# Optimization experiments

Measured on AMD Instinct MI355X. Metric: run time of the kernel, lower is better.

Reference implementation:

```python
import jax, jax.numpy as jnp
import numpy as np

N, C, H, W = 4, 128, 128, 128
G, K, PAD, DIL = 4, 3, 1, 1
P = K * K
HID = 4 * C
EPS = 1e-6


def ln(x, w, b):
    m = jnp.mean(x, -1, keepdims=True)
    v = jnp.mean((x - m) ** 2, -1, keepdims=True)
    return (x - m) * jax.lax.rsqrt(v + EPS) * w + b


def linear(x, w, b):
    return x @ w.T + b


def grid_sample_zeros(img, grid):
    # img: (B,Hi,Wi,Cc); grid: (B,L,P,2) xy in [-1,1]; bilinear, zeros padding, align_corners=False
    B, Hi, Wi, Cc = img.shape
    gx = (grid[..., 0] + 1.0) * (Wi * 0.5) - 0.5
    gy = (grid[..., 1] + 1.0) * (Hi * 0.5) - 0.5
    x0 = jnp.floor(gx)
    y0 = jnp.floor(gy)
    wx1 = gx - x0
    wy1 = gy - y0
    flat = img.reshape(B, Hi * Wi, Cc)
    Bq, L, Pq = gx.shape

    def tap(yy, xx, wgt):
        valid = (xx >= 0) & (xx <= Wi - 1) & (yy >= 0) & (yy <= Hi - 1)
        idx = (jnp.clip(yy, 0, Hi - 1) * Wi + jnp.clip(xx, 0, Wi - 1)).astype(jnp.int32)
        v = jnp.take_along_axis(flat, idx.reshape(B, L * Pq)[..., None], axis=1)
        return v.reshape(B, L, Pq, Cc) * (wgt * valid)[..., None]

    return (tap(y0, x0, (1 - wx1) * (1 - wy1))
            + tap(y0, x0 + 1, wx1 * (1 - wy1))
            + tap(y0 + 1, x0, (1 - wx1) * wy1)
            + tap(y0 + 1, x0 + 1, wx1 * wy1))


def dcn_core(x, offset, mask):
    # faithful port of dcnv3_core_pytorch (stride=1, offset_scale=1.0)
    n, h, w, c = x.shape
    gc = c // G
    xp = jnp.pad(x, ((0, 0), (PAD, PAD), (PAD, PAD), (0, 0)))
    hi, wi = h + 2 * PAD, w + 2 * PAD
    base = (DIL * (K - 1)) // 2 + 0.5
    ref_y = (base + jnp.arange(h, dtype=jnp.float32)) / hi
    ref_x = (base + jnp.arange(w, dtype=jnp.float32)) / wi
    ref = jnp.stack([jnp.broadcast_to(ref_x[None, :], (h, w)),
                     jnp.broadcast_to(ref_y[:, None], (h, w))], -1)  # (h,w,2) xy
    ks = jnp.arange(K, dtype=jnp.float32) * DIL - (DIL * (K - 1)) // 2
    gxk, gyk = jnp.meshgrid(ks, ks, indexing='ij')  # x slow, y fast (torch meshgrid order)
    grid = jnp.tile(jnp.stack([gxk / wi, gyk / hi], -1).reshape(P, 2), (G, 1))  # (G*P,2)
    sn = jnp.array([wi, hi], jnp.float32)
    loc = ref[None, :, :, None, :] + grid[None, None, None] + offset.reshape(n, h, w, G * P, 2) / sn
    sg = (2.0 * loc - 1.0).reshape(n, h * w, G, P, 2).transpose(0, 2, 1, 3, 4).reshape(n * G, h * w, P, 2)
    img = xp.reshape(n, hi, wi, G, gc).transpose(0, 3, 1, 2, 4).reshape(n * G, hi, wi, gc)
    samp = grid_sample_zeros(img, sg)  # (n*G, h*w, P, gc)
    m = mask.reshape(n, h * w, G, P).transpose(0, 2, 1, 3).reshape(n * G, h * w, P)
    out = jnp.einsum('blpc,blp->blc', samp, m)
    return out.reshape(n, G, h * w, gc).transpose(0, 2, 1, 3).reshape(n, h, w, c)


def dcn_forward(xcl, dw_w, dw_b, dwln_w, dwln_b, off_w, off_b, mask_w, mask_b, outproj_w, outproj_b):
    n, h, w, c = xcl.shape
    y = jax.lax.conv_general_dilated(xcl.transpose(0, 3, 1, 2), dw_w, (1, 1),
                                     ((PAD, PAD), (PAD, PAD)),
                                     dimension_numbers=('NCHW', 'OIHW', 'NCHW'),
                                     feature_group_count=C)
    y = y + dw_b[None, :, None, None]
    x1 = jax.nn.gelu(ln(y.transpose(0, 2, 3, 1), dwln_w, dwln_b), approximate=False)
    offset = linear(x1, off_w, off_b)
    m = jax.nn.softmax(linear(x1, mask_w, mask_b).reshape(n, h, w, G, P), -1).reshape(n, h, w, G * P)
    out = dcn_core(x1, offset, m)
    return linear(out, outproj_w, outproj_b)


def setup_inputs():
    key = jax.random.key(0)
    ks = jax.random.split(key, 8)
    s = 0.02
    return {
        "x": jax.random.normal(ks[0], (N, C, H, W), jnp.float32),
        "norm1_w": jnp.ones((C,), jnp.float32), "norm1_b": jnp.zeros((C,), jnp.float32),
        "dw_w": jax.random.normal(ks[1], (C, 1, K, K), jnp.float32) * 0.1,
        "dw_b": jnp.zeros((C,), jnp.float32),
        "dwln_w": jnp.ones((C,), jnp.float32), "dwln_b": jnp.zeros((C,), jnp.float32),
        "off_w": jax.random.normal(ks[2], (G * P * 2, C), jnp.float32) * 0.05,
        "off_b": jax.random.normal(ks[3], (G * P * 2,), jnp.float32) * 0.5,
        "mask_w": jax.random.normal(ks[4], (G * P, C), jnp.float32) * 0.05,
        "mask_b": jnp.zeros((G * P,), jnp.float32),
        "outproj_w": jax.random.normal(ks[5], (C, C), jnp.float32) * s,
        "outproj_b": jnp.zeros((C,), jnp.float32),
        "norm2_w": jnp.ones((C,), jnp.float32), "norm2_b": jnp.zeros((C,), jnp.float32),
        "fc1_w": jax.random.normal(ks[6], (HID, C), jnp.float32) * s,
        "fc1_b": jnp.zeros((HID,), jnp.float32),
        "fc2_w": jax.random.normal(ks[7], (C, HID), jnp.float32) * s,
        "fc2_b": jnp.zeros((C,), jnp.float32),
    }


def reference(x, norm1_w, norm1_b, dw_w, dw_b, dwln_w, dwln_b, off_w, off_b,
              mask_w, mask_b, outproj_w, outproj_b, norm2_w, norm2_b,
              fc1_w, fc1_b, fc2_w, fc2_b):
    # pre-norm branch (layer_scale=None, post_norm=False, res_post_norm=False, drop_path=Identity)
    xcl = ln(x.transpose(0, 2, 3, 1), norm1_w, norm1_b)  # channels_first -> channels_last LN
    d = dcn_forward(xcl, dw_w, dw_b, dwln_w, dwln_b, off_w, off_b, mask_w, mask_b, outproj_w, outproj_b)
    x = x + d.transpose(0, 3, 1, 2)
    y = ln(x.transpose(0, 2, 3, 1), norm2_w, norm2_b)
    y = linear(jax.nn.gelu(linear(y, fc1_w, fc1_b), approximate=False), fc2_w, fc2_b)
    return x + y.transpose(0, 3, 1, 2)
```

## Files before the change

kernel.cpp:

```cpp
#include <hip/hip_runtime.h>

typedef unsigned short ushort_t;
typedef short short8 __attribute__((ext_vector_type(8)));
typedef float f32x4 __attribute__((ext_vector_type(4)));
typedef ushort_t ushort8v __attribute__((ext_vector_type(8)));
typedef ushort_t ushort4v __attribute__((ext_vector_type(4)));

#define HWsz 16384
#define NHWsz 65536
#define YS 136

__device__ __forceinline__ float b2f(ushort_t u){ return __uint_as_float(((unsigned)u)<<16); }
__device__ __forceinline__ ushort_t f2b(float f){
  unsigned x = __float_as_uint(f);
  x += 0x7fffu + ((x>>16)&1u);
  return (ushort_t)(x>>16);
}
__device__ __forceinline__ float gelu_fast(float x){
  float t = x*x;
  float e = __expf(x*(1.5957691216f + 0.0713548163f*t));
  return x - x*__builtin_amdgcn_rcpf(1.0f + e);
}

#define HSW(p, b) ((p)*1024 + ((b) ^ (((p)&7)<<4)))
#define XSW(p, b) ((p)*256  + ((b) ^ (((p)&7)<<4)))

__global__ __launch_bounds__(256) void kW_cvt(const float* __restrict__ w1, const float* __restrict__ w2,
    const float* __restrict__ offw, const float* __restrict__ maskw, const float* __restrict__ dww,
    const float* __restrict__ pw, const float* __restrict__ offb, const float* __restrict__ mb,
    ushort_t* __restrict__ w1b, ushort_t* __restrict__ w2b, ushort_t* __restrict__ owmb,
    float* __restrict__ dwwT, ushort_t* __restrict__ pwh, ushort_t* __restrict__ pwl,
    float* __restrict__ obm){
  int i = blockIdx.x*256 + threadIdx.x;
  w1b[i] = f2b(w1[i]);
  w2b[i] = f2b(w2[i]);
  if (i < 16384){
    int row = i >> 7, k = i & 127;
    float v = 0.f;
    if (row < 72) v = offw[row*128 + k];
    else if (row < 108) v = maskw[(row-72)*128 + k];
    owmb[i] = f2b(v);
    float pv = pw[i];
    ushort_t hi = f2b(pv);
    pwh[i] = hi;
    pwl[i] = f2b(pv - b2f(hi));
  }
  if (i < 1152){
    int k = i >> 7, c = i & 127;
    dwwT[i] = dww[c*9 + k];
  }
  if (i < 128){
    obm[i] = (i < 72) ? offb[i] : ((i < 108) ? mb[i-72] : 0.f);
  }
}

__global__ __launch_bounds__(256) void kA_ln1(const float* __restrict__ x,
    const float* __restrict__ w, const float* __restrict__ b,
    ushort_t* __restrict__ xcl){
  __shared__ float tile[128*66];
  __shared__ float psum[256], psq[256];
  __shared__ float ms[64], rs[64];
  int t = threadIdx.x;
  int pos0 = blockIdx.x * 64;
  int n = pos0 >> 14, hw0 = pos0 & 16383;
  const float* xb = x + (size_t)n*128*HWsz + hw0;
  for (int i=0;i<32;i++){
    int e = i*256+t;
    int c = e>>6, p = e&63;
    tile[c*66+p] = xb[(size_t)c*HWsz + p];
  }
  __syncthreads();
  {
    int part = t>>6, p = t&63;
    float s=0.f, q=0.f;
    for (int c=part*32; c<part*32+32; c++){ float v = tile[c*66+p]; s+=v; q+=v*v; }
    psum[part*64+p]=s; psq[part*64+p]=q;
  }
  __syncthreads();
  if (t<64){
    float s=psum[t]+psum[64+t]+psum[128+t]+psum[192+t];
    float q=psq[t]+psq[64+t]+psq[128+t]+psq[192+t];
    float m = s*(1.0f/128.0f);
    float v = q*(1.0f/128.0f)-m*m;
    ms[t]=m; rs[t]=rsqrtf(v+1e-6f);
  }
  __syncthreads();
  for (int i=0;i<32;i++){
    int e = i*256+t;
    int p = e>>7, c = e&127;
    float v = (tile[c*66+p]-ms[p])*rs[p]*w[c]+b[c];
    xcl[(size_t)(pos0+p)*128 + c] = f2b(v);
  }
}

__global__ __launch_bounds__(256) void kB_dw(const ushort_t* __restrict__ xcl,
    const float* __restrict__ dwwT, const float* __restrict__ dwb,
    const float* __restrict__ lnw, const float* __restrict__ lnb,
    ushort_t* __restrict__ x1){
  __shared__ float partS[16*17], partQ[16*17];
  __shared__ float ms[16], rs[16];
  int t = threadIdx.x;
  int pos0 = blockIdx.x*16;
  int n = pos0>>14, hw0 = pos0&16383, h = hw0>>7, w0 = hw0&127;
  int pp = t>>4, l = t&15, ch0 = l*8;
  int w = w0 + pp;
  float acc[8];
  {
    float4 b0 = *(const float4*)(dwb + ch0);
    float4 b1 = *(const float4*)(dwb + ch0 + 4);
    acc[0]=b0.x; acc[1]=b0.y; acc[2]=b0.z; acc[3]=b0.w;
    acc[4]=b1.x; acc[5]=b1.y; acc[6]=b1.z; acc[7]=b1.w;
  }
  #pragma unroll
  for (int kh=0; kh<3; kh++){
    int hy = h + kh - 1;
    if ((unsigned)hy < 128u){
      #pragma unroll
      for (int kw=0; kw<3; kw++){
        int wx = w + kw - 1;
        if ((unsigned)wx < 128u){
          ushort8v xv = *(const ushort8v*)(xcl + ((size_t)(n*16384 + hy*128 + wx))*128 + ch0);
          const float* wr = dwwT + (kh*3+kw)*128 + ch0;
          float4 w0v = *(const float4*)(wr);
          float4 w1v = *(const float4*)(wr+4);
          acc[0] += b2f(xv[0])*w0v.x; acc[1] += b2f(xv[1])*w0v.y;
          acc[2] += b2f(xv[2])*w0v.z; acc[3] += b2f(xv[3])*w0v.w;
          acc[4] += b2f(xv[4])*w1v.x; acc[5] += b2f(xv[5])*w1v.y;
          acc[6] += b2f(xv[6])*w1v.z; acc[7] += b2f(xv[7])*w1v.w;
        }
      }
    }
  }
  {
    float s=0.f, q=0.f;
    #pragma unroll
    for (int j=0;j<8;j++){ s+=acc[j]; q+=acc[j]*acc[j]; }
    partS[pp*17+l]=s; partQ[pp*17+l]=q;
  }
  __syncthreads();
  if (t<16){
    float s=0.f, q=0.f;
    for (int i=0;i<16;i++){ s += partS[t*17+i]; q += partQ[t*17+i]; }
    float m = s*(1.0f/128.0f);
    float var = q*(1.0f/128.0f) - m*m;
    ms[t]=m; rs[t]=rsqrtf(var+1e-6f);
  }
  __syncthreads();
  {
    float m = ms[pp], r = rs[pp];
    float4 lw0 = *(const float4*)(lnw + ch0);
    float4 lw1 = *(const float4*)(lnw + ch0 + 4);
    float4 lb0 = *(const float4*)(lnb + ch0);
    float4 lb1 = *(const float4*)(lnb + ch0 + 4);
    float lw[8] = {lw0.x,lw0.y,lw0.z,lw0.w,lw1.x,lw1.y,lw1.z,lw1.w};
    float lb[8] = {lb0.x,lb0.y,lb0.z,lb0.w,lb1.x,lb1.y,lb1.z,lb1.w};
    ushort8v o;
    #pragma unroll
    for (int j=0;j<8;j++){
      float v = (acc[j]-m)*r*lw[j]+lb[j];
      o[j] = f2b(gelu_fast(v));
    }
    *(ushort8v*)(x1 + (size_t)(pos0+pp)*128 + ch0) = o;
  }
}

#define RS 120
__global__ __launch_bounds__(256) void kCD_dcn(const ushort_t* __restrict__ x1,
    const ushort_t* __restrict__ owmb, const float* __restrict__ obm,
    ushort_t* __restrict__ dcnout){
  __shared__ __align__(16) ushort_t xLb[16*YS];
  __shared__ float raw[16*RS];
  __shared__ __align__(16) float descW[576*4];
  __shared__ __align__(16) int   descO[576*4];
  int t = threadIdx.x;
  int pos0 = blockIdx.x*16;
  int n = pos0>>14, hw0 = pos0&16383, h = hw0>>7, w0 = hw0&127;
  const size_t imgbase = (size_t)n*16384*128;

  *(ushort8v*)(xLb + (t>>4)*YS + (t&15)*8) = *(const ushort8v*)(x1 + (size_t)pos0*128 + t*8);
  __syncthreads();

  {
    int wave = t>>6, lane = t&63;
    int ma = lane&15, quad = lane>>4;
    short8 afrag[4];
    #pragma unroll
    for (int ks=0; ks<4; ks++)
      afrag[ks] = *(const short8*)(xLb + ma*YS + ks*32 + quad*8);
    f32x4 acc[2];
    acc[0] = (f32x4){0.f,0.f,0.f,0.f};
    acc[1] = (f32x4){0.f,0.f,0.f,0.f};
    #pragma unroll
    for (int tile=0; tile<2; tile++){
      const ushort_t* brow = owmb + (size_t)(wave*32 + tile*16 + ma)*128 + quad*8;
      #pragma unroll
      for (int ks=0; ks<4; ks++){
        short8 bfrag = *(const short8*)(brow + ks*32);
        acc[tile] = __builtin_amdgcn_mfma_f32_16x16x32_bf16(bfrag, afrag[ks], acc[tile], 0,0,0);
      }
    }
    #pragma unroll
    for (int tile=0; tile<2; tile++){
      int row0 = wave*32 + tile*16 + quad*4;
      if (row0 < 112){
        f32x4 bias4 = *(const f32x4*)(obm + row0);
        f32x4 o;
        #pragma unroll
        for (int r=0;r<4;r++) o[r] = acc[tile][r] + bias4[r];
        *(f32x4*)(raw + ma*RS + row0) = o;
      }
    }
  }
  __syncthreads();

  if (t < 64){
    int p = t>>2, g = t&3;
    float* mr = raw + p*RS + 72 + g*9;
    float mx = -1e30f;
    for (int q=0;q<9;q++) mx = fmaxf(mx, mr[q]);
    float e[9]; float ssum=0.f;
    for (int q=0;q<9;q++){ e[q]=expf(mr[q]-mx); ssum+=e[q]; }
    float inv = 1.0f/ssum;
    for (int q=0;q<9;q++) mr[q] = e[q]*inv;
  }
  __syncthreads();

  for (int it=0; it<3; it++){
    int tid = t + 256*it;
    if (tid < 576){
      int pp = tid/36, rem = tid - pp*36;
      int g = rem/9, p = rem - g*9;
      int i = p/3, j = p - i*3;
      float ox = raw[pp*RS + 2*(g*9+p)];
      float oy = raw[pp*RS + 2*(g*9+p)+1];
      float mval = raw[pp*RS + 72 + g*9 + p];
      float px = (float)(w0 + pp + i - 1) + ox;
      float py = (float)(h + j - 1) + oy;
      float fx0 = floorf(px), fy0 = floorf(py);
      int ix0 = (int)fx0, iy0 = (int)fy0;
      float fx = px - fx0, fy = py - fy0;
      float vx0 = ((unsigned)ix0     < 128u) ? 1.f : 0.f;
      float vx1 = ((unsigned)(ix0+1) < 128u) ? 1.f : 0.f;
      float vy0 = ((unsigned)iy0     < 128u) ? 1.f : 0.f;
      float vy1 = ((unsigned)(iy0+1) < 128u) ? 1.f : 0.f;
      int cx0 = min(max(ix0,0),127), cx1 = min(max(ix0+1,0),127);
      int cy0 = min(max(iy0,0),127), cy1 = min(max(iy0+1,0),127);
      float4 wv;
      wv.x = (1.f-fx)*(1.f-fy)*mval*vx0*vy0;
      wv.y = fx*(1.f-fy)*mval*vx1*vy0;
      wv.z = (1.f-fx)*fy*mval*vx0*vy1;
      wv.w = fx*fy*mval*vx1*vy1;
      int4 ov;
      ov.x = (cy0*128+cx0)*128;
      ov.y = (cy0*128+cx1)*128;
      ov.z = (cy1*128+cx0)*128;
      ov.w = (cy1*128+cx1)*128;
      *(float4*)(descW + tid*4) = wv;
      *(int4*)(descO + tid*4) = ov;
    }
  }
  __syncthreads();

  {
    int pp = t>>4, l = t&15;
    int ch0 = l*8, g = l>>2;
    const ushort_t* ib = x1 + imgbase + ch0;
    float acc[8];
    #pragma unroll
    for (int j=0;j<8;j++) acc[j]=0.f;
    int dbase = pp*36 + g*9;
    #pragma unroll
    for (int p=0;p<9;p++){
      float4 wv = *(const float4*)(descW + (dbase+p)*4);
      int4  ov = *(const int4*)(descO + (dbase+p)*4);
      ushort8v v00 = *(const ushort8v*)(ib + ov.x);
      ushort8v v10 = *(const ushort8v*)(ib + ov.y);
      ushort8v v01 = *(const ushort8v*)(ib + ov.z);
      ushort8v v11 = *(const ushort8v*)(ib + ov.w);
      #pragma unroll
      for (int j=0;j<8;j++){
        float s = wv.x*b2f(v00[j]) + wv.y*b2f(v10[j]) + wv.z*b2f(v01[j]) + wv.w*b2f(v11[j]);
        acc[j] += s;
      }
    }
    ushort8v outv;
    #pragma unroll
    for (int j=0;j<8;j++) outv[j] = f2b(acc[j]);
    *(ushort8v*)(dcnout + (size_t)(pos0+pp)*128 + ch0) = outv;
  }
}

__global__ __launch_bounds__(256, 4) void kEFG(const ushort_t* __restrict__ dcnout,
    const ushort_t* __restrict__ pwh, const ushort_t* __restrict__ pwl,
    const float* __restrict__ pb, const float* __restrict__ x,
    const float* __restrict__ n2w, const float* __restrict__ n2b,
    const ushort_t* __restrict__ w1b, const float* __restrict__ b1,
    const ushort_t* __restrict__ w2b, const float* __restrict__ b2,
    float* __restrict__ out){
  __shared__ __align__(16) char hidb[32*1024];
  __shared__ __align__(16) char xnb[32*256];
  float* partS = (float*)hidb;
  float* partQ = partS + 32*17;
  float* msh   = partQ + 32*17;
  float* rsh   = msh + 32;

  int t = threadIdx.x;
  int pos0 = blockIdx.x*32;
  int n = pos0>>14, hw0 = pos0&16383;
  int wave = t>>6, lane = t&63;
  int ma = lane&15, quad = lane>>4;

  short8 af[2][4];
  #pragma unroll
  for (int mt=0; mt<2; mt++)
    #pragma unroll
    for (int ks=0; ks<4; ks++)
      af[mt][ks] = *(const short8*)(dcnout + (size_t)(pos0+mt*16+ma)*128 + ks*32 + quad*8);

  f32x4 acc[2][2];
  #pragma unroll
  for (int i=0;i<2;i++){ acc[i][0]=(f32x4){0.f,0.f,0.f,0.f}; acc[i][1]=(f32x4){0.f,0.f,0.f,0.f}; }
  #pragma unroll
  for (int tile=0; tile<2; tile++){
    int c0 = wave*32 + tile*16;
    const ushort_t* bh = pwh + (size_t)(c0 + ma)*128 + quad*8;
    const ushort_t* bl = pwl + (size_t)(c0 + ma)*128 + quad*8;
    #pragma unroll
    for (int ks=0; ks<4; ks++){
      short8 bfh = *(const short8*)(bh + ks*32);
      short8 bfl = *(const short8*)(bl + ks*32);
      #pragma unroll
      for (int mt=0; mt<2; mt++){
        acc[tile][mt] = __builtin_amdgcn_mfma_f32_16x16x32_bf16(bfh, af[mt][ks], acc[tile][mt], 0,0,0);
        acc[tile][mt] = __builtin_amdgcn_mfma_f32_16x16x32_bf16(bfl, af[mt][ks], acc[tile][mt], 0,0,0);
      }
    }
  }

  float vb[2][2][4];
  float sAcc[2], qAcc[2];
  sAcc[0]=0.f; sAcc[1]=0.f; qAcc[0]=0.f; qAcc[1]=0.f;
  #pragma unroll
  for (int tile=0; tile<2; tile++){
    int c0 = wave*32 + tile*16 + quad*4;
    f32x4 bias4 = *(const f32x4*)(pb + c0);
    #pragma unroll
    for (int mt=0; mt<2; mt++){
      int p = mt*16 + ma;
      #pragma unroll
      for (int r=0;r<4;r++){
        float res = x[((size_t)(n*128) + c0 + r)*HWsz + hw0 + p];
        float v = acc[tile][mt][r] + bias4[r] + res;
        float vv = b2f(f2b(v));
        vb[tile][mt][r] = vv;
        sAcc[mt] += vv; qAcc[mt] += vv*vv;
      }
    }
  }
  #pragma unroll
  for (int mt=0; mt<2; mt++){
    int p = mt*16 + ma;
    partS[p*17 + wave*4 + quad] = sAcc[mt];
    partQ[p*17 + wave*4 + quad] = qAcc[mt];
  }
  __syncthreads();
  if (t < 32){
    float s=0.f, q=0.f;
    for (int i=0;i<16;i++){ s += partS[t*17+i]; q += partQ[t*17+i]; }
    float m = s*(1.0f/128.0f);
    float var = q*(1.0f/128.0f) - m*m;
    msh[t] = m; rsh[t] = rsqrtf(var+1e-6f);
  }
  __syncthreads();

  #pragma unroll
  for (int tile=0; tile<2; tile++){
    int c0 = wave*32 + tile*16 + quad*4;
    f32x4 w4 = *(const f32x4*)(n2w + c0);
    f32x4 b4 = *(const f32x4*)(n2b + c0);
    #pragma unroll
    for (int mt=0; mt<2; mt++){
      int p = mt*16 + ma;
      float m = msh[p], r = rsh[p];
      ushort4v nv;
      #pragma unroll
      for (int rr=0;rr<4;rr++) nv[rr] = f2b((vb[tile][mt][rr]-m)*r*w4[rr] + b4[rr]);
      *(ushort4v*)(xnb + XSW(p, c0*2)) = nv;
    }
  }
  __syncthreads();

  short8 axf[2][4];
  #pragma unroll
  for (int ks=0; ks<4; ks++)
    #pragma unroll
    for (int mt=0; mt<2; mt++)
      axf[mt][ks] = *(const short8*)(xnb + XSW(mt*16+ma, ks*64 + quad*16));

  int nbase = wave*128;
  short8 wcur[4], wnxt[4];
  {
    const ushort_t* brow = w1b + (size_t)(nbase + ma)*128 + quad*8;
    #pragma unroll
    for (int ks=0; ks<4; ks++) wcur[ks] = *(const short8*)(brow + ks*32);
  }
  #pragma unroll
  for (int tile=0; tile<8; tile++){
    if (tile < 7){
      const ushort_t* brow = w1b + (size_t)(nbase + (tile+1)*16 + ma)*128 + quad*8;
      #pragma unroll
      for (int ks=0; ks<4; ks++) wnxt[ks] = *(const short8*)(brow + ks*32);
    }
    f32x4 a0 = (f32x4){0.f,0.f,0.f,0.f};
    f32x4 a1 = (f32x4){0.f,0.f,0.f,0.f};
    #pragma unroll
    for (int ks=0; ks<4; ks++){
      a0 = __builtin_amdgcn_mfma_f32_16x16x32_bf16(wcur[ks], axf[0][ks], a0, 0,0,0);
      a1 = __builtin_amdgcn_mfma_f32_16x16x32_bf16(wcur[ks], axf[1][ks], a1, 0,0,0);
    }
    int n0 = nbase + tile*16 + quad*4;
    f32x4 bias4 = *(const f32x4*)(b1 + n0);
    ushort4v hv0, hv1;
    #pragma unroll
    for (int r=0;r<4;r++){
      hv0[r] = f2b(gelu_fast(a0[r] + bias4[r]));
      hv1[r] = f2b(gelu_fast(a1[r] + bias4[r]));
    }
    *(ushort4v*)(hidb + HSW(ma,    n0*2)) = hv0;
    *(ushort4v*)(hidb + HSW(16+ma, n0*2)) = hv1;
    #pragma unroll
    for (int ks=0; ks<4; ks++) wcur[ks] = wnxt[ks];
  }
  __syncthreads();

  f32x4 acc2[2][2];
  acc2[0][0]=(f32x4){0.f,0.f,0.f,0.f}; acc2[0][1]=(f32x4){0.f,0.f,0.f,0.f};
  acc2[1][0]=(f32x4){0.f,0.f,0.f,0.f}; acc2[1][1]=(f32x4){0.f,0.f,0.f,0.f};
  const ushort_t* wb0 = w2b + (size_t)(wave*32 + ma)*512 + quad*8;
  const ushort_t* wb1 = w2b + (size_t)(wave*32 + 16 + ma)*512 + quad*8;
  short8 hc0 = *(const short8*)(hidb + HSW(ma,    quad*16));
  short8 hc1 = *(const short8*)(hidb + HSW(16+ma, quad*16));
  short8 wc0 = *(const short8*)(wb0);
  short8 wc1 = *(const short8*)(wb1);
  #pragma unroll
  for (int ks=0; ks<16; ks++){
    short8 hn0, hn1, wn0, wn1;
    if (ks < 15){
      hn0 = *(const short8*)(hidb + HSW(ma,    (ks+1)*64 + quad*16));
      hn1 = *(const short8*)(hidb + HSW(16+ma, (ks+1)*64 + quad*16));
      wn0 = *(const short8*)(wb0 + (ks+1)*32);
      wn1 = *(const short8*)(wb1 + (ks+1)*32);
    }
    acc2[0][0] = __builtin_amdgcn_mfma_f32_16x16x32_bf16(wc0, hc0, acc2[0][0], 0,0,0);
    acc2[0][1] = __builtin_amdgcn_mfma_f32_16x16x32_bf16(wc0, hc1, acc2[0][1], 0,0,0);
    acc2[1][0] = __builtin_amdgcn_mfma_f32_16x16x32_bf16(wc1, hc0, acc2[1][0], 0,0,0);
    acc2[1][1] = __builtin_amdgcn_mfma_f32_16x16x32_bf16(wc1, hc1, acc2[1][1], 0,0,0);
    if (ks < 15){ hc0=hn0; hc1=hn1; wc0=wn0; wc1=wn1; }
  }

  #pragma unroll
  for (int tile=0; tile<2; tile++){
    int c0 = wave*32 + tile*16 + quad*4;
    f32x4 bias4 = *(const f32x4*)(b2 + c0);
    #pragma unroll
    for (int mt=0; mt<2; mt++){
      int p = mt*16 + ma;
      #pragma unroll
      for (int r=0;r<4;r++){
        float v = acc2[tile][mt][r] + bias4[r] + vb[tile][mt][r];
        out[((size_t)(n*128) + c0 + r)*HWsz + hw0 + p] = v;
      }
    }
  }
}

extern "C" void kernel_launch(void* const* d_in, const int* in_sizes, int n_in,
                              void* d_out, int out_size, void* d_ws, size_t ws_size,
                              hipStream_t stream){
  const float* x     = (const float*)d_in[0];
  const float* n1w   = (const float*)d_in[1];
  const float* n1b   = (const float*)d_in[2];
  const float* dww   = (const float*)d_in[3];
  const float* dwb   = (const float*)d_in[4];
  const float* dwlnw = (const float*)d_in[5];
  const float* dwlnb = (const float*)d_in[6];
  const float* offw  = (const float*)d_in[7];
  const float* offb  = (const float*)d_in[8];
  const float* maskw = (const float*)d_in[9];
  const float* maskb = (const float*)d_in[10];
  const float* pw    = (const float*)d_in[11];
  const float* pb    = (const float*)d_in[12];
  const float* n2w   = (const float*)d_in[13];
  const float* n2b   = (const float*)d_in[14];
  const float* w1    = (const float*)d_in[15];
  const float* b1    = (const float*)d_in[16];
  const float* w2    = (const float*)d_in[17];
  const float* b2    = (const float*)d_in[18];

  char* wsb = (char*)d_ws;
  ushort_t* R0   = (ushort_t*)(wsb);
  ushort_t* R1   = (ushort_t*)(wsb + (16u<<20));
  ushort_t* w1b  = (ushort_t*)(wsb + (32u<<20));
  ushort_t* w2b  = (ushort_t*)(wsb + (32u<<20) + (128u<<10));
  ushort_t* owmb = (ushort_t*)(wsb + (32u<<20) + (256u<<10));
  ushort_t* pwh  = (ushort_t*)(wsb + (32u<<20) + (288u<<10));
  ushort_t* pwl  = (ushort_t*)(wsb + (32u<<20) + (320u<<10));
  float*    dwwT = (float*)(wsb + (32u<<20) + (352u<<10));
  float*    obm  = (float*)(wsb + (32u<<20) + (358u<<10));
  float* out = (float*)d_out;

  hipLaunchKernelGGL(kW_cvt,  dim3(256),   dim3(256), 0, stream, w1, w2, offw, maskw, dww, pw, offb, maskb, w1b, w2b, owmb, dwwT, pwh, pwl, obm);
  hipLaunchKernelGGL(kA_ln1,  dim3(1024),  dim3(256), 0, stream, x, n1w, n1b, R0);
  hipLaunchKernelGGL(kB_dw,   dim3(4096),  dim3(256), 0, stream, R0, dwwT, dwb, dwlnw, dwlnb, R1);
  hipLaunchKernelGGL(kCD_dcn, dim3(4096),  dim3(256), 0, stream, R1, owmb, obm, R0);
  hipLaunchKernelGGL(kEFG,    dim3(2048),  dim3(256), 0, stream, R0, pwh, pwl, pb, x, n2w, n2b, w1b, b1, w2b, b2, out);
}
```

Before: 276.9 us.

## Deepen weight prefetch pipelines, hoist residual loads, and use shuffle-based LayerNorm reductions

The MLP kernel now prefetches fc1 weights two tiles ahead with a triple register buffer, and fc2 weights four k-steps ahead alongside a two-deep hidden-tile prefetch. Residual x loads are issued before the projection MFMAs so their latency overlaps compute. Both LayerNorm statistic reductions replace a serial loop on a few threads with parallel partial loads and warp xor-shuffles. This targets memory latency stalls at the cost of more live registers, which may lower occupancy.

```diff
diff --git a/kernel.cpp b/kernel.cpp
--- a/kernel.cpp
+++ b/kernel.cpp
@@ -138,12 +138,19 @@
     partS[pp*17+l]=s; partQ[pp*17+l]=q;
   }
   __syncthreads();
-  if (t<16){
-    float s=0.f, q=0.f;
-    for (int i=0;i<16;i++){ s += partS[t*17+i]; q += partQ[t*17+i]; }
-    float m = s*(1.0f/128.0f);
-    float var = q*(1.0f/128.0f) - m*m;
-    ms[t]=m; rs[t]=rsqrtf(var+1e-6f);
+  {
+    int p = t>>4, j = t&15;
+    float s = partS[p*17+j];
+    float q = partQ[p*17+j];
+    s += __shfl_xor(s, 1);  q += __shfl_xor(q, 1);
+    s += __shfl_xor(s, 2);  q += __shfl_xor(q, 2);
+    s += __shfl_xor(s, 4);  q += __shfl_xor(q, 4);
+    s += __shfl_xor(s, 8);  q += __shfl_xor(q, 8);
+    if (j == 0){
+      float m = s*(1.0f/128.0f);
+      float var = q*(1.0f/128.0f) - m*m;
+      ms[p]=m; rs[p]=rsqrtf(var+1e-6f);
+    }
   }
   __syncthreads();
   {
@@ -317,6 +324,19 @@
     for (int ks=0; ks<4; ks++)
       af[mt][ks] = *(const short8*)(dcnout + (size_t)(pos0+mt*16+ma)*128 + ks*32 + quad*8);
 
+  float res[2][2][4];
+  #pragma unroll
+  for (int tile=0; tile<2; tile++){
+    int c0 = wave*32 + tile*16 + quad*4;
+    #pragma unroll
+    for (int mt=0; mt<2; mt++){
+      int p = mt*16 + ma;
+      #pragma unroll
+      for (int r=0;r<4;r++)
+        res[tile][mt][r] = x[((size_t)(n*128) + c0 + r)*HWsz + hw0 + p];
+    }
+  }
+
   f32x4 acc[2][2];
   #pragma unroll
   for (int i=0;i<2;i++){ acc[i][0]=(f32x4){0.f,0.f,0.f,0.f}; acc[i][1]=(f32x4){0.f,0.f,0.f,0.f}; }
@@ -346,11 +366,9 @@
     f32x4 bias4 = *(const f32x4*)(pb + c0);
     #pragma unroll
     for (int mt=0; mt<2; mt++){
-      int p = mt*16 + ma;
       #pragma unroll
       for (int r=0;r<4;r++){
-        float res = x[((size_t)(n*128) + c0 + r)*HWsz + hw0 + p];
-        float v = acc[tile][mt][r] + bias4[r] + res;
+        float v = acc[tile][mt][r] + bias4[r] + res[tile][mt][r];
         float vv = b2f(f2b(v));
         vb[tile][mt][r] = vv;
         sAcc[mt] += vv; qAcc[mt] += vv*vv;
@@ -364,12 +382,18 @@
     partQ[p*17 + wave*4 + quad] = qAcc[mt];
   }
   __syncthreads();
-  if (t < 32){
-    float s=0.f, q=0.f;
-    for (int i=0;i<16;i++){ s += partS[t*17+i]; q += partQ[t*17+i]; }
-    float m = s*(1.0f/128.0f);
-    float var = q*(1.0f/128.0f) - m*m;
-    msh[t] = m; rsh[t] = rsqrtf(var+1e-6f);
+  {
+    int p = t>>3, j = t&7;
+    float s = partS[p*17 + 2*j] + partS[p*17 + 2*j + 1];
+    float q = partQ[p*17 + 2*j] + partQ[p*17 + 2*j + 1];
+    s += __shfl_xor(s, 1);  q += __shfl_xor(q, 1);
+    s += __shfl_xor(s, 2);  q += __shfl_xor(q, 2);
+    s += __shfl_xor(s, 4);  q += __shfl_xor(q, 4);
+    if (j == 0){
+      float m = s*(1.0f/128.0f);
+      float var = q*(1.0f/128.0f) - m*m;
+      msh[p] = m; rsh[p] = rsqrtf(var+1e-6f);
+    }
   }
   __syncthreads();
 
@@ -398,25 +422,26 @@
       axf[mt][ks] = *(const short8*)(xnb + XSW(mt*16+ma, ks*64 + quad*16));
 
   int nbase = wave*128;
-  short8 wcur[4], wnxt[4];
-  {
-    const ushort_t* brow = w1b + (size_t)(nbase + ma)*128 + quad*8;
-    #pragma unroll
-    for (int ks=0; ks<4; ks++) wcur[ks] = *(const short8*)(brow + ks*32);
-  }
+  const ushort_t* w1base = w1b + (size_t)(nbase + ma)*128 + quad*8;
+  short8 wr[3][4];
+  #pragma unroll
+  for (int tt=0; tt<2; tt++)
+    #pragma unroll
+    for (int ks=0; ks<4; ks++)
+      wr[tt][ks] = *(const short8*)(w1base + tt*2048 + ks*32);
   #pragma unroll
   for (int tile=0; tile<8; tile++){
-    if (tile < 7){
-      const ushort_t* brow = w1b + (size_t)(nbase + (tile+1)*16 + ma)*128 + quad*8;
-      #pragma unroll
-      for (int ks=0; ks<4; ks++) wnxt[ks] = *(const short8*)(brow + ks*32);
+    if (tile < 6){
+      #pragma unroll
+      for (int ks=0; ks<4; ks++)
+        wr[(tile+2)%3][ks] = *(const short8*)(w1base + (tile+2)*2048 + ks*32);
     }
     f32x4 a0 = (f32x4){0.f,0.f,0.f,0.f};
     f32x4 a1 = (f32x4){0.f,0.f,0.f,0.f};
     #pragma unroll
     for (int ks=0; ks<4; ks++){
-      a0 = __builtin_amdgcn_mfma_f32_16x16x32_bf16(wcur[ks], axf[0][ks], a0, 0,0,0);
-      a1 = __builtin_amdgcn_mfma_f32_16x16x32_bf16(wcur[ks], axf[1][ks], a1, 0,0,0);
+      a0 = __builtin_amdgcn_mfma_f32_16x16x32_bf16(wr[tile%3][ks], axf[0][ks], a0, 0,0,0);
+      a1 = __builtin_amdgcn_mfma_f32_16x16x32_bf16(wr[tile%3][ks], axf[1][ks], a1, 0,0,0);
     }
     int n0 = nbase + tile*16 + quad*4;
     f32x4 bias4 = *(const f32x4*)(b1 + n0);
@@ -428,8 +453,6 @@
     }
     *(ushort4v*)(hidb + HSW(ma,    n0*2)) = hv0;
     *(ushort4v*)(hidb + HSW(16+ma, n0*2)) = hv1;
-    #pragma unroll
-    for (int ks=0; ks<4; ks++) wcur[ks] = wnxt[ks];
   }
   __syncthreads();
 
@@ -437,25 +460,34 @@
   acc2[0][0]=(f32x4){0.f,0.f,0.f,0.f}; acc2[0][1]=(f32x4){0.f,0.f,0.f,0.f};
   acc2[1][0]=(f32x4){0.f,0.f,0.f,0.f}; acc2[1][1]=(f32x4){0.f,0.f,0.f,0.f};
   const ushort_t* wb0 = w2b + (size_t)(wave*32 + ma)*512 + quad*8;
-  const ushort_t* wb1 = w2b + (size_t)(wave*32 + 16 + ma)*512 + quad*8;
-  short8 hc0 = *(const short8*)(hidb + HSW(ma,    quad*16));
-  short8 hc1 = *(const short8*)(hidb + HSW(16+ma, quad*16));
-  short8 wc0 = *(const short8*)(wb0);
-  short8 wc1 = *(const short8*)(wb1);
+  const ushort_t* wb1 = wb0 + 16*512;
+  short8 wq0[4], wq1[4];
+  #pragma unroll
+  for (int i=0;i<4;i++){
+    wq0[i] = *(const short8*)(wb0 + i*32);
+    wq1[i] = *(const short8*)(wb1 + i*32);
+  }
+  short8 hq0[2], hq1[2];
+  hq0[0] = *(const short8*)(hidb + HSW(ma,    quad*16));
+  hq1[0] = *(const short8*)(hidb + HSW(16+ma, quad*16));
+  hq0[1] = *(const short8*)(hidb + HSW(ma,    64 + quad*16));
+  hq1[1] = *(const short8*)(hidb + HSW(16+ma, 64 + quad*16));
   #pragma unroll
   for (int ks=0; ks<16; ks++){
-    short8 hn0, hn1, wn0, wn1;
-    if (ks < 15){
-      hn0 = *(const short8*)(hidb + HSW(ma,    (ks+1)*64 + quad*16));
-      hn1 = *(const short8*)(hidb + HSW(16+ma, (ks+1)*64 + quad*16));
-      wn0 = *(const short8*)(wb0 + (ks+1)*32);
-      wn1 = *(const short8*)(wb1 + (ks+1)*32);
+    short8 wc0 = wq0[ks&3], wc1 = wq1[ks&3];
+    short8 hc0 = hq0[ks&1], hc1 = hq1[ks&1];
+    if (ks < 12){
+      wq0[ks&3] = *(const short8*)(wb0 + (ks+4)*32);
+      wq1[ks&3] = *(const short8*)(wb1 + (ks+4)*32);
+    }
+    if (ks < 14){
+      hq0[ks&1] = *(const short8*)(hidb + HSW(ma,    (ks+2)*64 + quad*16));
+      hq1[ks&1] = *(const short8*)(hidb + HSW(16+ma, (ks+2)*64 + quad*16));
     }
     acc2[0][0] = __builtin_amdgcn_mfma_f32_16x16x32_bf16(wc0, hc0, acc2[0][0], 0,0,0);
     acc2[0][1] = __builtin_amdgcn_mfma_f32_16x16x32_bf16(wc0, hc1, acc2[0][1], 0,0,0);
     acc2[1][0] = __builtin_amdgcn_mfma_f32_16x16x32_bf16(wc1, hc0, acc2[1][0], 0,0,0);
     acc2[1][1] = __builtin_amdgcn_mfma_f32_16x16x32_bf16(wc1, hc1, acc2[1][1], 0,0,0);
-    if (ks < 15){ hc0=hn0; hc1=hn1; wc0=wn0; wc1=wn1; }
   }
 
   #pragma unroll
```

After: 277.9 us. Within noise of the previous version (+0.4%).
